# Kernel optimization log

Hardware: AMD Instinct MI355X
Metric: run time of the kernel (lower is better)

Reference implementation:

```python
import jax, jax.numpy as jnp
import numpy as np

T, B, I, H = 512, 256, 128, 256

def setup_inputs() -> dict:
    key = jax.random.key(0)
    ks = jax.random.split(key, 8)
    s_ih = 1.0 / np.sqrt(H)
    return {
        "x": jax.random.normal(ks[0], (T, B, I), dtype=jnp.float32),
        "gt": jax.random.uniform(ks[1], (T, B, 1), dtype=jnp.float32),
        "W_ih": jax.random.uniform(ks[2], (3 * H, I), minval=-s_ih, maxval=s_ih, dtype=jnp.float32),
        "W_hh": jax.random.uniform(ks[3], (3 * H, H), minval=-s_ih, maxval=s_ih, dtype=jnp.float32),
        "b_ih": jax.random.uniform(ks[4], (3 * H,), minval=-s_ih, maxval=s_ih, dtype=jnp.float32),
        "b_hh": jax.random.uniform(ks[5], (3 * H,), minval=-s_ih, maxval=s_ih, dtype=jnp.float32),
        "W_dec": jax.random.uniform(ks[6], (1, H), minval=-s_ih, maxval=s_ih, dtype=jnp.float32),
        "b_dec": jax.random.uniform(ks[7], (1,), minval=-s_ih, maxval=s_ih, dtype=jnp.float32),
    }

def reference(x, gt, W_ih, W_hh, b_ih, b_hh, W_dec, b_dec):
    h_dim = W_hh.shape[1]

    def step(h, inp):
        xt, gtt = inp  # xt: [B, I], gtt: [B, 1]
        gi = xt @ W_ih.T + b_ih          # [B, 3H]
        gh = h @ W_hh.T + b_hh           # [B, 3H]
        i_r, i_z, i_n = jnp.split(gi, 3, axis=-1)
        h_r, h_z, h_n = jnp.split(gh, 3, axis=-1)
        r = jax.nn.sigmoid(i_r + h_r)
        z = jax.nn.sigmoid(i_z + h_z)
        n = jnp.tanh(i_n + r * h_n)
        h_new = (1.0 - z) * n + z * h    # [B, H]
        logit = h_new @ W_dec.T + b_dec  # [B, 1]
        # BCE(sigmoid(logit), gt), reduction='sum': stable log-sigmoid form
        loss = -jnp.sum(gtt * jax.nn.log_sigmoid(logit)
                        + (1.0 - gtt) * jax.nn.log_sigmoid(-logit))
        return h_new, loss

    h0 = jnp.zeros((x.shape[1], h_dim), dtype=x.dtype)
    _, losses = jax.lax.scan(step, h0, (x[:-1], gt[1:]))
    return jnp.sum(losses)
```

## Files before the change

### kernel.cpp

```cpp
#include <hip/hip_runtime.h>
#include <hip/hip_bf16.h>


typedef __bf16 bf16x8_t __attribute__((ext_vector_type(8)));
typedef float floatx4_t __attribute__((ext_vector_type(4)));
typedef int intx4_t __attribute__((ext_vector_type(4)));
typedef unsigned int u32;
typedef u32 u32x4_t __attribute__((ext_vector_type(4)));

#define SW 2032.0f
#define SH 127.0f
#define INV_S (1.0f / (127.0f * 2032.0f))
#define NL2E (-1.44269504088896f)
#define CRZ (NL2E * INV_S)
#define CN (2.0f * NL2E * INV_S)

static __device__ inline u32 pack2bf(float a, float b) {
  __bf16 x = (__bf16)a, y = (__bf16)b;
  unsigned short ux = *(unsigned short*)&x, uy = *(unsigned short*)&y;
  return (u32)ux | ((u32)uy << 16);
}

__global__ void prep_kernel(const float* __restrict__ Whh,
                            const float* __restrict__ Wdec,
                            const float* __restrict__ Wih,
                            char* __restrict__ Wq, char* __restrict__ wdq,
                            __bf16* __restrict__ Wihb,
                            float* __restrict__ h_ws, float* __restrict__ out) {
  int idx = blockIdx.x * 256 + threadIdx.x;
  for (int i = idx; i < 768 * 256; i += 65536) {
    int v = (int)rintf(Whh[i] * SW);
    v = v > 127 ? 127 : (v < -127 ? -127 : v);
    Wq[i] = (char)v;
  }
  for (int i = idx; i < 768 * 128; i += 65536) Wihb[i] = (__bf16)Wih[i];
  if (idx < 256) {
    int v = (int)rintf(Wdec[idx] * SW);
    v = v > 127 ? 127 : (v < -127 ? -127 : v);
    wdq[idx] = (char)v;
  }
  if (idx < 65536) h_ws[idx] = 0.f;
  if (idx == 0) out[0] = 0.f;
}

__global__ __launch_bounds__(256) void xconv_kernel(const float* __restrict__ x,
                                                    __bf16* __restrict__ xb) {
  const size_t i = ((size_t)blockIdx.x * 256 + threadIdx.x) * 8;
  floatx4_t a = *(const floatx4_t*)(x + i);
  floatx4_t b = *(const floatx4_t*)(x + i + 4);
  bf16x8_t t;
#pragma unroll
  for (int j = 0; j < 4; ++j) {
    t[j] = (__bf16)a[j];
    t[4 + j] = (__bf16)b[j];
  }
  *(bf16x8_t*)(xb + i) = t;
}

__global__ __launch_bounds__(256, 2) void gemm2_kernel(
    const __bf16* __restrict__ xb,
    const __bf16* __restrict__ Wihb,
    const float* __restrict__ bih, const float* __restrict__ bhh,
    u32* __restrict__ giw, int tc) {
  const int tid = threadIdx.x;
  const int w = tid >> 6, lane = tid & 63;
  const int q = lane >> 4, nh = lane & 15;
  const int n0 = blockIdx.x * 128;
  const int wm = w >> 1, wn = w & 1;

  bf16x8_t af[4][4];
#pragma unroll
  for (int mt = 0; mt < 4; ++mt)
#pragma unroll
    for (int kk = 0; kk < 4; ++kk)
      af[mt][kk] = *(const bf16x8_t*)(Wihb +
                                      (size_t)(n0 + wm * 64 + mt * 16 + nh) *
                                          128 +
                                      kk * 32 + q * 8);

  const int gate = n0 >> 8;
  const float sc = (gate < 2) ? NL2E : (2.0f * NL2E);
  const int wr_base = ((n0 & 255) >> 5) + wm * 2;
  floatx4_t biasA[2], biasB[2];
#pragma unroll
  for (int a = 0; a < 2; ++a) {
    const int nnA = n0 + wm * 64 + a * 32 + q * 4;
    biasA[a] = *(const floatx4_t*)(bih + nnA);
    biasB[a] = *(const floatx4_t*)(bih + nnA + 16);
    if (gate < 2) {
      floatx4_t c1 = *(const floatx4_t*)(bhh + nnA);
      floatx4_t c2 = *(const floatx4_t*)(bhh + nnA + 16);
#pragma unroll
      for (int j = 0; j < 4; ++j) {
        biasA[a][j] += c1[j];
        biasB[a][j] += c2[j];
      }
    }
  }

  const int ntiles = tc * 2;
#pragma unroll 1
  for (int it = 0; it < 8; ++it) {
    const int bt = blockIdx.y * 8 + it;
    if (bt >= ntiles) break;
    const int ts = bt >> 1, b0 = (bt & 1) * 128;

    floatx4_t acc[4][4];
#pragma unroll
    for (int a = 0; a < 4; ++a)
#pragma unroll
      for (int b = 0; b < 4; ++b)
#pragma unroll
        for (int j = 0; j < 4; ++j) acc[a][b][j] = 0.f;

#pragma unroll
    for (int kk = 0; kk < 4; ++kk) {
      bf16x8_t bf[4];
#pragma unroll
      for (int nt = 0; nt < 4; ++nt)
        bf[nt] = *(const bf16x8_t*)(xb +
                                    (size_t)(ts * 256 + b0 + wn * 64 +
                                             nt * 16 + nh) *
                                        128 +
                                    kk * 32 + q * 8);
#pragma unroll
      for (int mt = 0; mt < 4; ++mt)
#pragma unroll
        for (int nt = 0; nt < 4; ++nt)
          acc[mt][nt] = __builtin_amdgcn_mfma_f32_16x16x32_bf16(
              af[mt][kk], bf[nt], acc[mt][nt], 0, 0, 0);
    }

#pragma unroll
    for (int a = 0; a < 2; ++a) {
      const int wrec = wr_base + a;
#pragma unroll
      for (int nt = 0; nt < 4; ++nt) {
        const int bb = b0 + wn * 64 + nt * 16 + nh;
        const int gg = bb >> 2, jb = bb & 3;
        size_t U = (((size_t)ts * 64 + gg) * 3 + gate) * 512 + wrec * 64 +
                   jb * 16 + q * 4;
        u32x4_t pv;
#pragma unroll
        for (int j = 0; j < 4; ++j)
          pv[j] = pack2bf((acc[2 * a][nt][j] + biasA[a][j]) * sc,
                          (acc[2 * a + 1][nt][j] + biasB[a][j]) * sc);
        *(u32x4_t*)(giw + U) = pv;
      }
    }
  }
}

__global__ __launch_bounds__(1024) void rec_kernel(
    const char* __restrict__ Wq,
    const char* __restrict__ wdq,
    const u32* __restrict__ gi,
    const float* __restrict__ gt, const float* __restrict__ bdec,
    const float* __restrict__ bhh, float* __restrict__ h_ws,
    float* __restrict__ out, int t0, int tc) {
  __shared__ char hb[2][4][288];
  __shared__ float lp[4][2048];

  const int tid = threadIdx.x;
  const int w = tid >> 6, lane = tid & 63;
  const int q = lane >> 4, nh = lane & 15;
  const int g = blockIdx.x;
  const int col = w * 16 + nh;
  const int wp = w >> 1;
  const int hi = w & 1;

  intx4_t wf[3][4];
#pragma unroll
  for (int c = 0; c < 3; ++c) {
    const int n = c * 256 + col;
#pragma unroll
    for (int kb = 0; kb < 4; ++kb)
      wf[c][kb] = *(const intx4_t*)(Wq + (size_t)n * 256 + kb * 64 + q * 16);
  }
  intx4_t wdfk;
  {
    const int kb = (w >= 12) ? (w - 12) : 0;
    intx4_t z = {0, 0, 0, 0};
    intx4_t v = *(const intx4_t*)(wdq + kb * 64 + q * 16);
    wdfk = (nh == 0) ? v : z;
  }

  const float bn2 = 2.0f * NL2E * bhh[512 + col];
  const float bdec0 = bdec[0];

  if (tid < 256) {
    const int rr = tid >> 6, c0 = (tid & 63) * 4;
    u32 p = 0;
#pragma unroll
    for (int j = 0; j < 4; ++j) {
      int a = (int)rintf(h_ws[(size_t)(g * 4 + rr) * 256 + c0 + j] * SH);
      a = a > 127 ? 127 : (a < -127 ? -127 : a);
      p |= ((u32)(a & 255)) << (8 * j);
    }
    *(u32*)&hb[0][rr][c0] = p;
  }
  float ho = h_ws[(size_t)(g * 4 + q) * 256 + col];
  __syncthreads();

  const int tcm1 = tc - 1;
  const size_t boff = (size_t)wp * 64 + q * 16 + nh;
  u32 GA[3], GB[3];
  {
    size_t u0 = ((size_t)g * 3) * 512 + boff;
#pragma unroll
    for (int c = 0; c < 3; ++c) GA[c] = gi[u0 + c * 512];
    const int t1s = tc > 1 ? 1 : 0;
    size_t u1 = (((size_t)t1s * 64 + g) * 3) * 512 + boff;
#pragma unroll
    for (int c = 0; c < 3; ++c) GB[c] = gi[u1 + c * 512];
  }

  auto STEP = [&](int T, u32* G, int TPRE) {
    const int pb = T & 1;
    intx4_t hbf[4];
#pragma unroll
    for (int kb = 0; kb < 4; ++kb)
      hbf[kb] = *(const intx4_t*)&hb[pb][nh >> 2][kb * 64 + q * 16];

    float gv0, gv1, gv2;
    if (hi) {
      gv0 = __uint_as_float(G[0] & 0xffff0000u);
      gv1 = __uint_as_float(G[1] & 0xffff0000u);
      gv2 = __uint_as_float(G[2] & 0xffff0000u);
    } else {
      gv0 = __uint_as_float(G[0] << 16);
      gv1 = __uint_as_float(G[1] << 16);
      gv2 = __uint_as_float(G[2] << 16);
    }
    {
      size_t up = (((size_t)TPRE * 64 + g) * 3) * 512 + boff;
#pragma unroll
      for (int c = 0; c < 3; ++c) G[c] = gi[up + c * 512];
    }

    intx4_t acc[3];
#pragma unroll
    for (int cs = 0; cs < 3; ++cs)
#pragma unroll
      for (int jj = 0; jj < 4; ++jj) acc[cs][jj] = 0;

#pragma unroll
    for (int kb = 0; kb < 4; ++kb)
#pragma unroll
      for (int cs = 0; cs < 3; ++cs)
        acc[cs] = __builtin_amdgcn_mfma_i32_16x16x64_i8(hbf[kb], wf[cs][kb],
                                                        acc[cs], 0, 0, 0);

    if (w >= 12) {
      intx4_t hsel = (w == 12) ? hbf[0]
                   : (w == 13) ? hbf[1]
                   : (w == 14) ? hbf[2] : hbf[3];
      intx4_t facc = {0, 0, 0, 0};
      facc = __builtin_amdgcn_mfma_i32_16x16x64_i8(hsel, wdfk, facc, 0, 0, 0);
      if (nh == 0 && T >= 1) lp[w - 12][(T - 1) * 4 + q] = (float)facc[0];
    }

    float rr0 = __builtin_amdgcn_rcpf(
        1.f + __builtin_amdgcn_exp2f((float)acc[0][0] * CRZ + gv0));
    float zz0 = __builtin_amdgcn_rcpf(
        1.f + __builtin_amdgcn_exp2f((float)acc[1][0] * CRZ + gv1));
    float hn2 = (float)acc[2][0] * CN + bn2;
    float tv0 = 2.f * __builtin_amdgcn_rcpf(
                          1.f + __builtin_amdgcn_exp2f(rr0 * hn2 + gv2)) -
                1.f;
    float hnew = tv0 + zz0 * (ho - tv0);
    ho = hnew;
    int h8 = (int)rintf(hnew * SH);
    hb[1 - pb][q][col] = (char)h8;

    asm volatile("s_waitcnt lgkmcnt(0)" ::: "memory");
    __builtin_amdgcn_s_barrier();
    asm volatile("" ::: "memory");
  };

  int t = 0;
#pragma unroll 1
  for (; t + 1 < tc; t += 2) {
    STEP(t, GA, (t + 2 <= tcm1) ? t + 2 : tcm1);
    STEP(t + 1, GB, (t + 3 <= tcm1) ? t + 3 : tcm1);
  }
  if (t < tc) STEP(t, GA, tcm1);

  if (w >= 12) {
    const int kb = w - 12;
    intx4_t b = *(const intx4_t*)&hb[tc & 1][nh >> 2][kb * 64 + q * 16];
    intx4_t fac2 = {0, 0, 0, 0};
    fac2 = __builtin_amdgcn_mfma_i32_16x16x64_i8(b, wdfk, fac2, 0, 0, 0);
    if (nh == 0) lp[kb][(tc - 1) * 4 + q] = (float)fac2[0];
  }
  __syncthreads();

  float loss = 0.f;
  for (int i = tid; i < tc * 4; i += 1024) {
    float l = (lp[0][i] + lp[1][i] + lp[2][i] + lp[3][i]) * INV_S + bdec0;
    float gtv = gt[(size_t)(t0 + (i >> 2) + 1) * 256 + g * 4 + (i & 3)];
    float t1 = log1pf(__expf(-fabsf(l)));
    loss += gtv * (fmaxf(-l, 0.f) + t1) + (1.f - gtv) * (fmaxf(l, 0.f) + t1);
  }
  loss += __shfl_xor(loss, 1);
  loss += __shfl_xor(loss, 2);
  loss += __shfl_xor(loss, 4);
  loss += __shfl_xor(loss, 8);
  loss += __shfl_xor(loss, 16);
  loss += __shfl_xor(loss, 32);
  if (lane == 0) atomicAdd(out, loss);

  h_ws[(size_t)(g * 4 + q) * 256 + col] = ho;
}

extern "C" void kernel_launch(void* const* d_in, const int* in_sizes, int n_in,
                              void* d_out, int out_size, void* d_ws,
                              size_t ws_size, hipStream_t stream) {
  const float* x = (const float*)d_in[0];
  const float* gt = (const float*)d_in[1];
  const float* Wih = (const float*)d_in[2];
  const float* Whh = (const float*)d_in[3];
  const float* bih = (const float*)d_in[4];
  const float* bhh = (const float*)d_in[5];
  const float* Wdec = (const float*)d_in[6];
  const float* bdec = (const float*)d_in[7];
  float* out = (float*)d_out;

  char* ws = (char*)d_ws;
  char* Wq = ws;
  char* wdq = ws + 196608;
  float* h_ws = (float*)(ws + 197120);
  __bf16* Wihb = (__bf16*)(ws + 459264);
  char* dyn = ws + 655872;
  const size_t per_step = (size_t)393216 + 65536;
  size_t avail = ws_size > 655872 ? ws_size - 655872 : per_step;
  int Tc = (int)(avail / per_step);
  if (Tc < 1) Tc = 1;
  if (Tc > 511) Tc = 511;
  __bf16* xb = (__bf16*)dyn;
  u32* gi = (u32*)(dyn + (size_t)Tc * 65536);

  prep_kernel<<<256, 256, 0, stream>>>(Whh, Wdec, Wih, Wq, wdq, Wihb, h_ws,
                                       out);
  for (int t0 = 0; t0 < 511; t0 += Tc) {
    const int tc = (511 - t0 < Tc) ? (511 - t0) : Tc;
    xconv_kernel<<<tc * 16, 256, 0, stream>>>(x + (size_t)t0 * 256 * 128, xb);
    gemm2_kernel<<<dim3(6, (tc * 2 + 7) / 8), 256, 0, stream>>>(xb, Wihb, bih,
                                                                bhh, gi, tc);
    rec_kernel<<<64, 1024, 0, stream>>>(Wq, wdq, gi, gt, bdec, bhh, h_ws, out,
                                        t0, tc);
  }
}
```

Before: 523.7 us.

## Fuse prep and x conversion into the input-projection GEMM kernel

```diff
diff --git a/kernel.cpp b/kernel.cpp
--- a/kernel.cpp
+++ b/kernel.cpp
@@ -21,62 +21,57 @@
   return (u32)ux | ((u32)uy << 16);
 }
 
-__global__ void prep_kernel(const float* __restrict__ Whh,
-                            const float* __restrict__ Wdec,
-                            const float* __restrict__ Wih,
-                            char* __restrict__ Wq, char* __restrict__ wdq,
-                            __bf16* __restrict__ Wihb,
-                            float* __restrict__ h_ws, float* __restrict__ out) {
-  int idx = blockIdx.x * 256 + threadIdx.x;
-  for (int i = idx; i < 768 * 256; i += 65536) {
-    int v = (int)rintf(Whh[i] * SW);
-    v = v > 127 ? 127 : (v < -127 ? -127 : v);
-    Wq[i] = (char)v;
-  }
-  for (int i = idx; i < 768 * 128; i += 65536) Wihb[i] = (__bf16)Wih[i];
-  if (idx < 256) {
-    int v = (int)rintf(Wdec[idx] * SW);
-    v = v > 127 ? 127 : (v < -127 ? -127 : v);
-    wdq[idx] = (char)v;
-  }
-  if (idx < 65536) h_ws[idx] = 0.f;
-  if (idx == 0) out[0] = 0.f;
-}
-
-__global__ __launch_bounds__(256) void xconv_kernel(const float* __restrict__ x,
-                                                    __bf16* __restrict__ xb) {
-  const size_t i = ((size_t)blockIdx.x * 256 + threadIdx.x) * 8;
-  floatx4_t a = *(const floatx4_t*)(x + i);
-  floatx4_t b = *(const floatx4_t*)(x + i + 4);
+static __device__ inline bf16x8_t cvt8(const float* __restrict__ p) {
+  floatx4_t a = *(const floatx4_t*)p;
+  floatx4_t b = *(const floatx4_t*)(p + 4);
   bf16x8_t t;
 #pragma unroll
   for (int j = 0; j < 4; ++j) {
     t[j] = (__bf16)a[j];
     t[4 + j] = (__bf16)b[j];
   }
-  *(bf16x8_t*)(xb + i) = t;
-}
-
-__global__ __launch_bounds__(256, 2) void gemm2_kernel(
-    const __bf16* __restrict__ xb,
-    const __bf16* __restrict__ Wihb,
+  return t;
+}
+
+__global__ __launch_bounds__(256, 2) void gemm3_kernel(
+    const float* __restrict__ x,
+    const float* __restrict__ Wih,
     const float* __restrict__ bih, const float* __restrict__ bhh,
-    u32* __restrict__ giw, int tc) {
+    const float* __restrict__ Whh,
+    const float* __restrict__ Wdec,
+    char* __restrict__ Wq, char* __restrict__ wdq,
+    float* __restrict__ h_ws, u32* __restrict__ giw,
+    float* __restrict__ out, int first) {
   const int tid = threadIdx.x;
   const int w = tid >> 6, lane = tid & 63;
   const int q = lane >> 4, nh = lane & 15;
   const int n0 = blockIdx.x * 128;
   const int wm = w >> 1, wn = w & 1;
+  const int flat = blockIdx.y * 6 + blockIdx.x;
+  const int nthr = gridDim.y * 6 * 256;
+
+  for (int i = flat * 256 + tid; i < 768 * 256; i += nthr) {
+    int v = (int)rintf(Whh[i] * SW);
+    v = v > 127 ? 127 : (v < -127 ? -127 : v);
+    Wq[i] = (char)v;
+  }
+  if (flat == 0) {
+    int v = (int)rintf(Wdec[tid] * SW);
+    v = v > 127 ? 127 : (v < -127 ? -127 : v);
+    wdq[tid] = (char)v;
+  }
+  if (first) {
+    for (int i = flat * 256 + tid; i < 65536; i += nthr) h_ws[i] = 0.f;
+    if (flat == 0 && tid == 0) out[0] = 0.f;
+  }
 
   bf16x8_t af[4][4];
 #pragma unroll
   for (int mt = 0; mt < 4; ++mt)
 #pragma unroll
     for (int kk = 0; kk < 4; ++kk)
-      af[mt][kk] = *(const bf16x8_t*)(Wihb +
-                                      (size_t)(n0 + wm * 64 + mt * 16 + nh) *
-                                          128 +
-                                      kk * 32 + q * 8);
+      af[mt][kk] = cvt8(Wih + (size_t)(n0 + wm * 64 + mt * 16 + nh) * 128 +
+                        kk * 32 + q * 8);
 
   const int gate = n0 >> 8;
   const float sc = (gate < 2) ? NL2E : (2.0f * NL2E);
@@ -98,55 +93,47 @@
     }
   }
 
-  const int ntiles = tc * 2;
-#pragma unroll 1
-  for (int it = 0; it < 8; ++it) {
-    const int bt = blockIdx.y * 8 + it;
-    if (bt >= ntiles) break;
-    const int ts = bt >> 1, b0 = (bt & 1) * 128;
-
-    floatx4_t acc[4][4];
-#pragma unroll
-    for (int a = 0; a < 4; ++a)
-#pragma unroll
-      for (int b = 0; b < 4; ++b)
-#pragma unroll
-        for (int j = 0; j < 4; ++j) acc[a][b][j] = 0.f;
-
-#pragma unroll
-    for (int kk = 0; kk < 4; ++kk) {
-      bf16x8_t bf[4];
+  const int ts = blockIdx.y >> 1;
+  const int b0 = (blockIdx.y & 1) * 128;
+
+  floatx4_t acc[4][4];
+#pragma unroll
+  for (int a = 0; a < 4; ++a)
+#pragma unroll
+    for (int b = 0; b < 4; ++b)
+#pragma unroll
+      for (int j = 0; j < 4; ++j) acc[a][b][j] = 0.f;
+
+#pragma unroll
+  for (int kk = 0; kk < 4; ++kk) {
+    bf16x8_t bf[4];
+#pragma unroll
+    for (int nt = 0; nt < 4; ++nt)
+      bf[nt] = cvt8(x + (size_t)(ts * 256 + b0 + wn * 64 + nt * 16 + nh) * 128 +
+                    kk * 32 + q * 8);
+#pragma unroll
+    for (int mt = 0; mt < 4; ++mt)
 #pragma unroll
       for (int nt = 0; nt < 4; ++nt)
-        bf[nt] = *(const bf16x8_t*)(xb +
-                                    (size_t)(ts * 256 + b0 + wn * 64 +
-                                             nt * 16 + nh) *
-                                        128 +
-                                    kk * 32 + q * 8);
-#pragma unroll
-      for (int mt = 0; mt < 4; ++mt)
-#pragma unroll
-        for (int nt = 0; nt < 4; ++nt)
-          acc[mt][nt] = __builtin_amdgcn_mfma_f32_16x16x32_bf16(
-              af[mt][kk], bf[nt], acc[mt][nt], 0, 0, 0);
-    }
-
-#pragma unroll
-    for (int a = 0; a < 2; ++a) {
-      const int wrec = wr_base + a;
-#pragma unroll
-      for (int nt = 0; nt < 4; ++nt) {
-        const int bb = b0 + wn * 64 + nt * 16 + nh;
-        const int gg = bb >> 2, jb = bb & 3;
-        size_t U = (((size_t)ts * 64 + gg) * 3 + gate) * 512 + wrec * 64 +
-                   jb * 16 + q * 4;
-        u32x4_t pv;
-#pragma unroll
-        for (int j = 0; j < 4; ++j)
-          pv[j] = pack2bf((acc[2 * a][nt][j] + biasA[a][j]) * sc,
-                          (acc[2 * a + 1][nt][j] + biasB[a][j]) * sc);
-        *(u32x4_t*)(giw + U) = pv;
-      }
+        acc[mt][nt] = __builtin_amdgcn_mfma_f32_16x16x32_bf16(
+            af[mt][kk], bf[nt], acc[mt][nt], 0, 0, 0);
+  }
+
+#pragma unroll
+  for (int a = 0; a < 2; ++a) {
+    const int wrec = wr_base + a;
+#pragma unroll
+    for (int nt = 0; nt < 4; ++nt) {
+      const int bb = b0 + wn * 64 + nt * 16 + nh;
+      const int gg = bb >> 2, jb = bb & 3;
+      size_t U = (((size_t)ts * 64 + gg) * 3 + gate) * 512 + wrec * 64 +
+                 jb * 16 + q * 4;
+      u32x4_t pv;
+#pragma unroll
+      for (int j = 0; j < 4; ++j)
+        pv[j] = pack2bf((acc[2 * a][nt][j] + biasA[a][j]) * sc,
+                        (acc[2 * a + 1][nt][j] + biasB[a][j]) * sc);
+      *(u32x4_t*)(giw + U) = pv;
     }
   }
 }
@@ -330,23 +317,19 @@
   char* Wq = ws;
   char* wdq = ws + 196608;
   float* h_ws = (float*)(ws + 197120);
-  __bf16* Wihb = (__bf16*)(ws + 459264);
-  char* dyn = ws + 655872;
-  const size_t per_step = (size_t)393216 + 65536;
-  size_t avail = ws_size > 655872 ? ws_size - 655872 : per_step;
+  char* dyn = ws + 459264;
+  const size_t per_step = (size_t)393216;
+  size_t avail = ws_size > 459264 ? ws_size - 459264 : per_step;
   int Tc = (int)(avail / per_step);
   if (Tc < 1) Tc = 1;
   if (Tc > 511) Tc = 511;
-  __bf16* xb = (__bf16*)dyn;
-  u32* gi = (u32*)(dyn + (size_t)Tc * 65536);
-
-  prep_kernel<<<256, 256, 0, stream>>>(Whh, Wdec, Wih, Wq, wdq, Wihb, h_ws,
-                                       out);
+  u32* gi = (u32*)dyn;
+
   for (int t0 = 0; t0 < 511; t0 += Tc) {
     const int tc = (511 - t0 < Tc) ? (511 - t0) : Tc;
-    xconv_kernel<<<tc * 16, 256, 0, stream>>>(x + (size_t)t0 * 256 * 128, xb);
-    gemm2_kernel<<<dim3(6, (tc * 2 + 7) / 8), 256, 0, stream>>>(xb, Wihb, bih,
-                                                                bhh, gi, tc);
+    gemm3_kernel<<<dim3(6, tc * 2), 256, 0, stream>>>(
+        x + (size_t)t0 * 256 * 128, Wih, bih, bhh, Whh, Wdec, Wq, wdq, h_ws,
+        gi, out, t0 == 0 ? 1 : 0);
     rec_kernel<<<64, 1024, 0, stream>>>(Wq, wdq, gi, gt, bdec, bhh, h_ws, out,
                                         t0, tc);
   }
```

New measurement: 625.8 us. 19.5% more time.
